# Kernel tuning notes

Hardware: AMD Instinct MI355X
Metric: run time of the kernel (lower is better)

## Reference

```python
import jax, jax.numpy as jnp
import numpy as np

N_NODES = 100000
N_EDGES = 3200000
N_GRAPHS = 4096
BN_EPS = 1e-5


def setup_inputs() -> dict:
    key = jax.random.key(0)
    ks = iter(jax.random.split(key, 64))
    d = {}
    d["x"] = jax.random.normal(next(ks), (N_NODES, 36), dtype=jnp.float32)
    d["edge_index"] = jax.random.randint(next(ks), (2, N_EDGES), 0, N_NODES, dtype=jnp.int32)
    d["batch"] = jnp.sort(jax.random.randint(next(ks), (N_NODES,), 0, N_GRAPHS, dtype=jnp.int32))
    d["num_graphs"] = N_GRAPHS
    # GCN layers: (in, out) per hidden_dims=[128,128,64]
    dims = [(36, 128), (128, 128), (128, 64)]
    for i, (di, do) in enumerate(dims):
        d[f"w{i}"] = jax.random.normal(next(ks), (di, do), dtype=jnp.float32) * (1.0 / np.sqrt(di))
        d[f"b{i}"] = jax.random.normal(next(ks), (do,), dtype=jnp.float32) * 0.01
        d[f"g{i}"] = jax.random.uniform(next(ks), (do,), dtype=jnp.float32, minval=0.5, maxval=1.5)
        d[f"be{i}"] = jax.random.normal(next(ks), (do,), dtype=jnp.float32) * 0.01
        d[f"m{i}"] = jax.random.normal(next(ks), (do,), dtype=jnp.float32) * 0.01
        d[f"v{i}"] = jax.random.uniform(next(ks), (do,), dtype=jnp.float32, minval=0.5, maxval=1.5)
    # FC head: 64 -> 128 -> 64 -> 2
    d["fw0"] = jax.random.normal(next(ks), (64, 128), dtype=jnp.float32) * (1.0 / 8.0)
    d["fb0"] = jax.random.normal(next(ks), (128,), dtype=jnp.float32) * 0.01
    d["fw1"] = jax.random.normal(next(ks), (128, 64), dtype=jnp.float32) * (1.0 / np.sqrt(128))
    d["fb1"] = jax.random.normal(next(ks), (64,), dtype=jnp.float32) * 0.01
    d["ow"] = jax.random.normal(next(ks), (64, 2), dtype=jnp.float32) * (1.0 / 8.0)
    d["ob"] = jax.random.normal(next(ks), (2,), dtype=jnp.float32) * 0.01
    return d


def _gcn_layer(x, w, b, src, dst, norm_e, norm_self, n_nodes):
    # PyG GCNConv with self-loops: out[i] = sum_j norm_ij * (x_j @ W) + b
    xw = x @ w                                   # [N, out]
    msg = xw[src] * norm_e[:, None]              # gather + scale, [E, out]
    agg = jax.ops.segment_sum(msg, dst, num_segments=n_nodes)
    return agg + xw * norm_self[:, None] + b     # self-loop contribution + bias


def _bn_eval(x, g, be, m, v):
    return g * (x - m) * jax.lax.rsqrt(v + BN_EPS) + be


def reference(x, edge_index, batch, num_graphs,
              w0, b0, g0, be0, m0, v0,
              w1, b1, g1, be1, m1, v1,
              w2, b2, g2, be2, m2, v2,
              fw0, fb0, fw1, fb1, ow, ob):
    n = x.shape[0]
    src, dst = edge_index[0], edge_index[1]
    # symmetric GCN normalization with self-loops (gcn_norm)
    deg = jax.ops.segment_sum(jnp.ones(src.shape[0], x.dtype), dst, num_segments=n) + 1.0
    dinv = jax.lax.rsqrt(deg)
    norm_e = dinv[src] * dinv[dst]   # per-edge coeff
    norm_self = dinv * dinv          # self-loop coeff = 1/deg

    params = [(w0, b0, g0, be0, m0, v0), (w1, b1, g1, be1, m1, v1), (w2, b2, g2, be2, m2, v2)]
    h = x
    for (w, b, g, be, m, v) in params:
        h = _gcn_layer(h, w, b, src, dst, norm_e, norm_self, n)
        h = jax.nn.relu(_bn_eval(h, g, be, m, v))  # dropout inactive in eval

    # global mean pool over graphs
    sums = jax.ops.segment_sum(h, batch, num_segments=num_graphs)          # [G, 64]
    cnt = jax.ops.segment_sum(jnp.ones(n, h.dtype), batch, num_segments=num_graphs)
    pooled = sums / jnp.maximum(cnt, 1.0)[:, None]

    h = jax.nn.relu(pooled @ fw0 + fb0)
    h = jax.nn.relu(h @ fw1 + fb1)
    return h @ ow + ob
```

## Files before the change

kernel.cpp:

```cpp
#include <hip/hip_runtime.h>
#include <hip/hip_fp16.h>

#define BN_EPS 1e-5f

#define BUCK_SHIFT 9
#define NBUCK_MAX 256
#define BCAP 20480
#define PBLK 512

typedef _Float16 f16x8 __attribute__((ext_vector_type(8)));
typedef float f32x4 __attribute__((ext_vector_type(4)));

__global__ __launch_bounds__(256) void fused_scatter(const int* __restrict__ src,
                                                     const int* __restrict__ dst,
                                                     int* __restrict__ gcnt,
                                                     int2* __restrict__ ebuf,
                                                     int nE, int nbuck, int chunk) {
    __shared__ int h[NBUCK_MAX], rbase[NBUCK_MAX], cur[NBUCK_MAX];
    const int blk = blockIdx.x, tid = threadIdx.x;
    for (int j = tid; j < nbuck; j += 256) { h[j] = 0; cur[j] = 0; }
    __syncthreads();
    const int base = blk * chunk;
    const int end = min(base + chunk, nE);
    for (int i = base + tid; i < end; i += 256)
        atomicAdd(&h[dst[i] >> BUCK_SHIFT], 1);
    __syncthreads();
    for (int j = tid; j < nbuck; j += 256)
        rbase[j] = h[j] ? atomicAdd(&gcnt[j], h[j]) : 0;
    __syncthreads();
    for (int i = base + tid; i < end; i += 256) {
        int s = src[i], d = dst[i];
        int b = d >> BUCK_SHIFT;
        int p = rbase[b] + atomicAdd(&cur[b], 1);
        if (p < BCAP) ebuf[(size_t)b * BCAP + p] = make_int2(s, d);
    }
}

__global__ __launch_bounds__(256) void fused_csr(const int2* __restrict__ ebuf,
                                                 const int* __restrict__ gcnt,
                                                 const float* __restrict__ x,
                                                 const int* __restrict__ batch,
                                                 int* __restrict__ degI,
                                                 float* __restrict__ dinv,
                                                 int* __restrict__ row_start,
                                                 int* __restrict__ src_sorted,
                                                 __half* __restrict__ xs_h,
                                                 float* __restrict__ cnt, int n) {
    __shared__ int deg[512];
    __shared__ int cur[512];
    __shared__ float sdi[512];
    __shared__ int tmp[256];
    __shared__ int s_low_total;
    const int b = blockIdx.x, tid = threadIdx.x;
    const int nb = b << BUCK_SHIFT;
    const int cntb = min(gcnt[b], BCAP);
    const int2* __restrict__ eb = ebuf + (size_t)b * BCAP;

    for (int j = tid; j < 512; j += 256) deg[j] = 0;
    __syncthreads();
    for (int i = tid; i < cntb; i += 256)
        atomicAdd(&deg[eb[i].y - nb], 1);
    __syncthreads();

    for (int j = tid; j < 512; j += 256) {
        int node = nb + j;
        if (node < n) {
            int d = deg[j];
            degI[node] = d;
            float di = rsqrtf((float)d + 1.0f);
            dinv[node] = di;
            sdi[j] = di;
        }
    }

    int v0 = deg[tid];
    tmp[tid] = v0;
    __syncthreads();
    for (int off = 1; off < 256; off <<= 1) {
        int t = (tid >= off) ? tmp[tid - off] : 0;
        __syncthreads();
        tmp[tid] += t;
        __syncthreads();
    }
    int ex_low = tmp[tid] - v0;
    if (tid == 255) s_low_total = tmp[255];
    __syncthreads();
    int low_total = s_low_total;
    int v1 = deg[256 + tid];
    __syncthreads();
    tmp[tid] = v1;
    __syncthreads();
    for (int off = 1; off < 256; off <<= 1) {
        int t = (tid >= off) ? tmp[tid - off] : 0;
        __syncthreads();
        tmp[tid] += t;
        __syncthreads();
    }
    int ex_high = tmp[tid] - v1 + low_total;

    const int gbase = b * BCAP;
    if (nb + tid < n) row_start[nb + tid] = gbase + ex_low;
    if (nb + 256 + tid < n) row_start[nb + 256 + tid] = gbase + ex_high;
    cur[tid] = ex_low;
    cur[256 + tid] = ex_high;
    __syncthreads();

    for (int i = tid; i < cntb; i += 256) {
        int2 ed = eb[i];
        int p = atomicAdd(&cur[ed.y - nb], 1);
        src_sorted[gbase + p] = ed.x;
    }

    for (int idx = tid; idx < 512 * 18; idx += 256) {
        int j = idx / 18;
        int node = nb + j;
        if (node < n) {
            int c = idx - j * 18;
            float2 v = *(const float2*)(x + (size_t)node * 36 + 2 * c);
            float di = sdi[j];
            *(__half2*)(xs_h + (size_t)node * 36 + 2 * c) = __floats2half2_rn(v.x * di, v.y * di);
        }
    }

    for (int j = tid; j < 512; j += 256) {
        int node = nb + j;
        if (node < n) unsafeAtomicAdd(&cnt[batch[node]], 1.0f);
    }
}

__global__ __launch_bounds__(256) void repack_w(const float* __restrict__ w0,
                                                const float* __restrict__ w1,
                                                const float* __restrict__ w2,
                                                __half* __restrict__ Wp0,
                                                __half* __restrict__ Wp1,
                                                __half* __restrict__ Wp2) {
    const int tid = threadIdx.x;
    if (blockIdx.x == 0) {
        for (int idx = tid; idx < 8 * 4 * 64 * 8; idx += 256) {
            int j = idx & 7, lane = (idx >> 3) & 63, kb = (idx >> 9) & 3, nt = idx >> 11;
            int k = kb * 32 + (lane >> 4) * 8 + j, c = nt * 16 + (lane & 15);
            Wp1[idx] = __float2half_rn(w1[k * 128 + c]);
        }
    } else if (blockIdx.x == 1) {
        for (int idx = tid; idx < 4 * 4 * 64 * 8; idx += 256) {
            int j = idx & 7, lane = (idx >> 3) & 63, kb = (idx >> 9) & 3, nt = idx >> 11;
            int k = kb * 32 + (lane >> 4) * 8 + j, c = nt * 16 + (lane & 15);
            Wp2[idx] = __float2half_rn(w2[k * 64 + c]);
        }
    } else {
        for (int idx = tid; idx < 8 * 2 * 64 * 8; idx += 256) {
            int j = idx & 7, lane = (idx >> 3) & 63, kb = (idx >> 9) & 1, nt = idx >> 10;
            int k = kb * 32 + (lane >> 4) * 8 + j, c = nt * 16 + (lane & 15);
            Wp0[idx] = (k < 36) ? __float2half_rn(w0[k * 128 + c]) : __float2half_rn(0.0f);
        }
    }
}

template<int LDK, int KB, int OUT, int NT, bool BNRELU, bool SCALEOUT>
__global__ __launch_bounds__(256) void gemm_mfma(const __half* __restrict__ in,
                                                 const __half* __restrict__ Wp,
                                                 const float* __restrict__ bias,
                                                 const float* __restrict__ gg,
                                                 const float* __restrict__ bb,
                                                 const float* __restrict__ mm,
                                                 const float* __restrict__ vv,
                                                 const float* __restrict__ dscale,
                                                 __half* __restrict__ out, int n) {
    const int lane = threadIdx.x & 63;
    const int wave = threadIdx.x >> 6;
    const int r0 = blockIdx.x * 64 + wave * 16;
    const int arow = r0 + (lane & 15);
    const int kg = lane >> 4;

    f16x8 a[KB];
#pragma unroll
    for (int kb = 0; kb < KB; kb++)
        a[kb] = *(const f16x8*)(in + (size_t)arow * LDK + kb * 32 + kg * 8);

    f32x4 acc[NT];
#pragma unroll
    for (int nt = 0; nt < NT; nt++) {
        f32x4 z = {0.0f, 0.0f, 0.0f, 0.0f};
        acc[nt] = z;
    }

#pragma unroll
    for (int nt = 0; nt < NT; nt++) {
#pragma unroll
        for (int kb = 0; kb < KB; kb++) {
            f16x8 b = *(const f16x8*)(Wp + ((size_t)(nt * KB + kb) * 64 + lane) * 8);
            acc[nt] = __builtin_amdgcn_mfma_f32_16x16x32_f16(a[kb], b, acc[nt], 0, 0, 0);
        }
    }

    const int col = lane & 15;
    const int rbase = r0 + kg * 4;
    float ds[4] = {1.f, 1.f, 1.f, 1.f};
    if constexpr (SCALEOUT) {
#pragma unroll
        for (int r = 0; r < 4; r++) ds[r] = dscale[rbase + r];
    }
#pragma unroll
    for (int nt = 0; nt < NT; nt++) {
        const int c = nt * 16 + col;
        float s = 1.f, t = 0.f;
        if constexpr (BNRELU) {
            s = gg[c] * rsqrtf(vv[c] + BN_EPS);
            t = bb[c] + (bias[c] - mm[c]) * s;
        }
#pragma unroll
        for (int r = 0; r < 4; r++) {
            float val = acc[nt][r];
            if constexpr (BNRELU) val = fmaxf(val * s + t, 0.0f);
            if constexpr (SCALEOUT) val *= ds[r];
            out[(size_t)(rbase + r) * OUT + c] = __float2half_rn(val);
        }
    }
}

__global__ __launch_bounds__(256) void agg_pull36w_h(const __half* __restrict__ xs_h,
                                                     const int* __restrict__ row_start,
                                                     const int* __restrict__ degI,
                                                     const int* __restrict__ src_sorted,
                                                     const float* __restrict__ dinv,
                                                     __half* __restrict__ out, int n) {
    int node = __builtin_amdgcn_readfirstlane((int)(blockIdx.x * 4 + (threadIdx.x >> 6)));
    if (node >= n) return;
    const int lane = threadIdx.x & 63;
    int e = row_start[node];
    const int re = e + degI[node];
    const float di = dinv[node];

    const char* __restrict__ xb = (const char*)xs_h;
    const unsigned loff = (unsigned)lane << 2;

    float2 acc = make_float2(0.f, 0.f);
    if (lane < 18) acc = __half22float2(*(const __half2*)(xb + ((unsigned)node * 72u + loff)));

    for (; e + 3 < re; e += 4) {
        int s0 = src_sorted[e], s1 = src_sorted[e + 1],
            s2 = src_sorted[e + 2], s3 = src_sorted[e + 3];
        if (lane < 18) {
            float2 a0 = __half22float2(*(const __half2*)(xb + ((unsigned)s0 * 72u + loff)));
            float2 a1 = __half22float2(*(const __half2*)(xb + ((unsigned)s1 * 72u + loff)));
            float2 a2 = __half22float2(*(const __half2*)(xb + ((unsigned)s2 * 72u + loff)));
            float2 a3 = __half22float2(*(const __half2*)(xb + ((unsigned)s3 * 72u + loff)));
            acc.x += (a0.x + a1.x) + (a2.x + a3.x);
            acc.y += (a0.y + a1.y) + (a2.y + a3.y);
        }
    }
    for (; e < re; e++) {
        int s = src_sorted[e];
        if (lane < 18) {
            float2 a = __half22float2(*(const __half2*)(xb + ((unsigned)s * 72u + loff)));
            acc.x += a.x;
            acc.y += a.y;
        }
    }
    if (lane < 32) {
        __half2 o = __floats2half2_rn(acc.x * di, acc.y * di);
        *(__half2*)((char*)out + (((unsigned)node << 7) + loff)) = o;
    }
}

__global__ __launch_bounds__(256) void agg_pull_wave2_h(const __half* __restrict__ feat_h,
                                                        const int* __restrict__ row_start,
                                                        const int* __restrict__ degI,
                                                        const int* __restrict__ src_sorted,
                                                        const float* __restrict__ dinv,
                                                        __half* __restrict__ out, int n) {
    int node = __builtin_amdgcn_readfirstlane((int)(blockIdx.x * 4 + (threadIdx.x >> 6)));
    if (node >= n) return;
    const int lane = threadIdx.x & 63;
    int e = row_start[node];
    const int re = e + degI[node];
    const float di = dinv[node];

    const char* __restrict__ fb = (const char*)feat_h;
    const unsigned loff = (unsigned)lane << 2;

    float2 acc = __half22float2(*(const __half2*)(fb + (((unsigned)node << 8) + loff)));

    for (; e + 3 < re; e += 4) {
        int s0 = src_sorted[e], s1 = src_sorted[e + 1],
            s2 = src_sorted[e + 2], s3 = src_sorted[e + 3];
        float2 a0 = __half22float2(*(const __half2*)(fb + (((unsigned)s0 << 8) + loff)));
        float2 a1 = __half22float2(*(const __half2*)(fb + (((unsigned)s1 << 8) + loff)));
        float2 a2 = __half22float2(*(const __half2*)(fb + (((unsigned)s2 << 8) + loff)));
        float2 a3 = __half22float2(*(const __half2*)(fb + (((unsigned)s3 << 8) + loff)));
        acc.x += (a0.x + a1.x) + (a2.x + a3.x);
        acc.y += (a0.y + a1.y) + (a2.y + a3.y);
    }
    for (; e < re; e++) {
        int s = src_sorted[e];
        float2 a = __half22float2(*(const __half2*)(fb + (((unsigned)s << 8) + loff)));
        acc.x += a.x;
        acc.y += a.y;
    }
    __half2 o = __floats2half2_rn(acc.x * di, acc.y * di);
    *(__half2*)((char*)out + (((unsigned)node << 8) + loff)) = o;
}

__global__ __launch_bounds__(256) void agg_pull_pool_h(const __half* __restrict__ feat_h,
                                                       const int* __restrict__ row_start,
                                                       const int* __restrict__ degI,
                                                       const int* __restrict__ src_sorted,
                                                       const float* __restrict__ dinv,
                                                       const float* __restrict__ bias,
                                                       const float* __restrict__ gg,
                                                       const float* __restrict__ bb,
                                                       const float* __restrict__ mm,
                                                       const float* __restrict__ vv,
                                                       const int* __restrict__ batch,
                                                       float* __restrict__ pool, int n) {
    int node = __builtin_amdgcn_readfirstlane((int)(blockIdx.x * 4 + (threadIdx.x >> 6)));
    if (node >= n) return;
    const int lane = threadIdx.x & 63;
    int e = row_start[node];
    const int re = e + degI[node];
    const float di = dinv[node];

    const char* __restrict__ fb = (const char*)feat_h;
    const unsigned loff = (unsigned)lane << 1;

    float acc = __half2float(*(const __half*)(fb + (((unsigned)node << 7) + loff)));

    for (; e + 3 < re; e += 4) {
        int s0 = src_sorted[e], s1 = src_sorted[e + 1],
            s2 = src_sorted[e + 2], s3 = src_sorted[e + 3];
        float a0 = __half2float(*(const __half*)(fb + (((unsigned)s0 << 7) + loff)));
        float a1 = __half2float(*(const __half*)(fb + (((unsigned)s1 << 7) + loff)));
        float a2 = __half2float(*(const __half*)(fb + (((unsigned)s2 << 7) + loff)));
        float a3 = __half2float(*(const __half*)(fb + (((unsigned)s3 << 7) + loff)));
        acc += (a0 + a1) + (a2 + a3);
    }
    for (; e < re; e++) {
        acc += __half2float(*(const __half*)(fb + (((unsigned)src_sorted[e] << 7) + loff)));
    }
    float h = acc * di + bias[lane];
    float scale = gg[lane] * rsqrtf(vv[lane] + BN_EPS);
    float val = fmaxf((h - mm[lane]) * scale + bb[lane], 0.0f);
    unsafeAtomicAdd(&pool[(size_t)batch[node] * 64 + lane], val);
}

__global__ __launch_bounds__(128) void fc_head_kernel(const float* __restrict__ pool,
                                                      const float* __restrict__ cnt,
                                                      const float* __restrict__ fw0,
                                                      const float* __restrict__ fb0,
                                                      const float* __restrict__ fw1,
                                                      const float* __restrict__ fb1,
                                                      const float* __restrict__ ow,
                                                      const float* __restrict__ ob,
                                                      float* __restrict__ out) {
    int g = blockIdx.x, tid = threadIdx.x;
    __shared__ float p[64], h1[128], h2[64];
    if (tid < 64) p[tid] = pool[g * 64 + tid] / fmaxf(cnt[g], 1.0f);
    __syncthreads();
    {
        float acc = fb0[tid];
        for (int k = 0; k < 64; k++) acc += p[k] * fw0[k * 128 + tid];
        h1[tid] = fmaxf(acc, 0.0f);
    }
    __syncthreads();
    if (tid < 64) {
        float acc = fb1[tid];
        for (int k = 0; k < 128; k++) acc += h1[k] * fw1[k * 64 + tid];
        h2[tid] = fmaxf(acc, 0.0f);
    }
    __syncthreads();
    if (tid < 2) {
        float acc = ob[tid];
        for (int k = 0; k < 64; k++) acc += h2[k] * ow[k * 2 + tid];
        out[g * 2 + tid] = acc;
    }
}

extern "C" void kernel_launch(void* const* d_in, const int* in_sizes, int n_in,
                              void* d_out, int out_size, void* d_ws, size_t ws_size,
                              hipStream_t stream) {
    const float* x     = (const float*)d_in[0];
    const int*   eidx  = (const int*)d_in[1];
    const int*   batch = (const int*)d_in[2];
    const float* w0 = (const float*)d_in[4];
    const float* b0 = (const float*)d_in[5];
    const float* g0 = (const float*)d_in[6];
    const float* be0 = (const float*)d_in[7];
    const float* m0 = (const float*)d_in[8];
    const float* v0 = (const float*)d_in[9];
    const float* w1 = (const float*)d_in[10];
    const float* b1 = (const float*)d_in[11];
    const float* g1 = (const float*)d_in[12];
    const float* be1 = (const float*)d_in[13];
    const float* m1 = (const float*)d_in[14];
    const float* v1 = (const float*)d_in[15];
    const float* w2 = (const float*)d_in[16];
    const float* b2 = (const float*)d_in[17];
    const float* g2 = (const float*)d_in[18];
    const float* be2 = (const float*)d_in[19];
    const float* m2 = (const float*)d_in[20];
    const float* v2 = (const float*)d_in[21];
    const float* fw0 = (const float*)d_in[22];
    const float* fb0 = (const float*)d_in[23];
    const float* fw1 = (const float*)d_in[24];
    const float* fb1 = (const float*)d_in[25];
    const float* ow = (const float*)d_in[26];
    const float* ob = (const float*)d_in[27];

    const int N = in_sizes[0] / 36;
    const int E = in_sizes[1] / 2;
    const int G = out_size / 2;
    const int* src = eidx;
    const int* dst = eidx + E;

    const int nbuck = (N + 511) >> BUCK_SHIFT;
    const int chunk = (E + PBLK - 1) / PBLK;
    const int NPAD = ((N + 63) / 64) * 64;
    const int NGP = NPAD / 64;

    char* wsb = (char*)d_ws;
    int2*   ebuf       = (int2*)wsb;    wsb += (size_t)nbuck * BCAP * 8;
    __half* F1         = (__half*)wsb;  wsb += (size_t)NPAD * 128 * 2;
    __half* F1a        = (__half*)wsb;  wsb += (size_t)NPAD * 128 * 2;
    __half* F2         = (__half*)wsb;  wsb += (size_t)NPAD * 64 * 2;
    __half* A36h       = (__half*)wsb;  wsb += (size_t)NPAD * 64 * 2;
    __half* xs_h       = (__half*)wsb;  wsb += (size_t)N * 36 * 2;
    int*    src_sorted = (int*)wsb;     wsb += (size_t)nbuck * BCAP * 4;
    int*    degI       = (int*)wsb;     wsb += (size_t)N * 4;
    int*    row_start  = (int*)wsb;     wsb += (size_t)N * 4;
    float*  dinv       = (float*)wsb;   wsb += (size_t)NPAD * 4;
    float*  pool       = (float*)wsb;   wsb += (size_t)G * 64 * 4;
    float*  cnt        = (float*)wsb;   wsb += (size_t)G * 4;
    int*    gcnt       = (int*)wsb;     wsb += 256 * 4;
    __half* Wp0        = (__half*)wsb;  wsb += 8192 * 2;
    __half* Wp1        = (__half*)wsb;  wsb += 16384 * 2;
    __half* Wp2        = (__half*)wsb;  wsb += 8192 * 2;
    __half* F1b        = (__half*)ebuf;

    hipMemsetAsync(gcnt, 0, 256 * 4, stream);
    hipMemsetAsync(pool, 0, (size_t)G * 64 * 4, stream);
    hipMemsetAsync(cnt, 0, (size_t)G * 4, stream);
    repack_w<<<3, 256, 0, stream>>>(w0, w1, w2, Wp0, Wp1, Wp2);

    fused_scatter<<<PBLK, 256, 0, stream>>>(src, dst, gcnt, ebuf, E, nbuck, chunk);
    fused_csr<<<nbuck, 256, 0, stream>>>(ebuf, gcnt, x, batch, degI, dinv, row_start,
                                         src_sorted, xs_h, cnt, N);

    const int NW = (N + 3) / 4;

    agg_pull36w_h<<<NW, 256, 0, stream>>>(xs_h, row_start, degI, src_sorted, dinv, A36h, N);
    gemm_mfma<64, 2, 128, 8, true, true><<<NGP, 256, 0, stream>>>(
        A36h, Wp0, b0, g0, be0, m0, v0, dinv, F1, N);

    agg_pull_wave2_h<<<NW, 256, 0, stream>>>(F1, row_start, degI, src_sorted, dinv, F1a, N);
    gemm_mfma<128, 4, 128, 8, true, false><<<NGP, 256, 0, stream>>>(
        F1a, Wp1, b1, g1, be1, m1, v1, nullptr, F1b, N);

    gemm_mfma<128, 4, 64, 4, false, true><<<NGP, 256, 0, stream>>>(
        F1b, Wp2, nullptr, nullptr, nullptr, nullptr, nullptr, dinv, F2, N);

    agg_pull_pool_h<<<NW, 256, 0, stream>>>(
        F2, row_start, degI, src_sorted, dinv, b2, g2, be2, m2, v2, batch, pool, N);

    fc_head_kernel<<<G, 128, 0, stream>>>(pool, cnt, fw0, fb0, fw1, fb1, ow, ob, (float*)d_out);
}
```

Before: 576.5 us.

## Fuse layer-1/2 GEMMs, pack edge buffer to 32-bit, merge prep memsets

Merges the layer-1 GEMM (with BN+ReLU) and the layer-2 GEMM into one kernel that keeps the intermediate 16x128 tile per wave in LDS, so the F1b round trip through global memory and one launch go away. The bucketed edge buffer now packs the local destination (9 bits) and the source (17 bits) into one int, which halves scatter write and CSR read traffic. The three memsets and the weight repack become a single prep kernel. Packing assumes node ids fit in 17 bits (N < 131072), which holds for this input size.

```diff
diff --git a/kernel.cpp b/kernel.cpp
--- a/kernel.cpp
+++ b/kernel.cpp
@@ -11,10 +11,50 @@
 typedef _Float16 f16x8 __attribute__((ext_vector_type(8)));
 typedef float f32x4 __attribute__((ext_vector_type(4)));
 
+__global__ __launch_bounds__(256) void prep0(const float* __restrict__ w0,
+                                             const float* __restrict__ w1,
+                                             const float* __restrict__ w2,
+                                             __half* __restrict__ Wp0,
+                                             __half* __restrict__ Wp1,
+                                             __half* __restrict__ Wp2,
+                                             int* __restrict__ gcnt,
+                                             float* __restrict__ pool,
+                                             float* __restrict__ cnt, int G) {
+    const int tid = threadIdx.x;
+    if (blockIdx.x == 0) {
+        for (int idx = tid; idx < 8 * 4 * 64 * 8; idx += 256) {
+            int j = idx & 7, lane = (idx >> 3) & 63, kb = (idx >> 9) & 3, nt = idx >> 11;
+            int k = kb * 32 + (lane >> 4) * 8 + j, c = nt * 16 + (lane & 15);
+            Wp1[idx] = __float2half_rn(w1[k * 128 + c]);
+        }
+    } else if (blockIdx.x == 1) {
+        for (int idx = tid; idx < 4 * 4 * 64 * 8; idx += 256) {
+            int j = idx & 7, lane = (idx >> 3) & 63, kb = (idx >> 9) & 3, nt = idx >> 11;
+            int k = kb * 32 + (lane >> 4) * 8 + j, c = nt * 16 + (lane & 15);
+            Wp2[idx] = __float2half_rn(w2[k * 64 + c]);
+        }
+    } else if (blockIdx.x == 2) {
+        for (int idx = tid; idx < 8 * 2 * 64 * 8; idx += 256) {
+            int j = idx & 7, lane = (idx >> 3) & 63, kb = (idx >> 9) & 1, nt = idx >> 10;
+            int k = kb * 32 + (lane >> 4) * 8 + j, c = nt * 16 + (lane & 15);
+            Wp0[idx] = (k < 36) ? __float2half_rn(w0[k * 128 + c]) : __float2half_rn(0.0f);
+        }
+    } else {
+        const int zb = blockIdx.x - 3;
+        const int nzb = gridDim.x - 3;
+        const int tot = G * 64 + G + 256;
+        for (int i = zb * 256 + tid; i < tot; i += nzb * 256) {
+            if (i < G * 64) pool[i] = 0.0f;
+            else if (i < G * 64 + G) cnt[i - G * 64] = 0.0f;
+            else gcnt[i - G * 64 - G] = 0;
+        }
+    }
+}
+
 __global__ __launch_bounds__(256) void fused_scatter(const int* __restrict__ src,
                                                      const int* __restrict__ dst,
                                                      int* __restrict__ gcnt,
-                                                     int2* __restrict__ ebuf,
+                                                     int* __restrict__ ebuf,
                                                      int nE, int nbuck, int chunk) {
     __shared__ int h[NBUCK_MAX], rbase[NBUCK_MAX], cur[NBUCK_MAX];
     const int blk = blockIdx.x, tid = threadIdx.x;
@@ -32,11 +72,11 @@
         int s = src[i], d = dst[i];
         int b = d >> BUCK_SHIFT;
         int p = rbase[b] + atomicAdd(&cur[b], 1);
-        if (p < BCAP) ebuf[(size_t)b * BCAP + p] = make_int2(s, d);
-    }
-}
-
-__global__ __launch_bounds__(256) void fused_csr(const int2* __restrict__ ebuf,
+        if (p < BCAP) ebuf[(size_t)b * BCAP + p] = ((d & 511) << 17) | s;
+    }
+}
+
+__global__ __launch_bounds__(256) void fused_csr(const int* __restrict__ ebuf,
                                                  const int* __restrict__ gcnt,
                                                  const float* __restrict__ x,
                                                  const int* __restrict__ batch,
@@ -54,12 +94,12 @@
     const int b = blockIdx.x, tid = threadIdx.x;
     const int nb = b << BUCK_SHIFT;
     const int cntb = min(gcnt[b], BCAP);
-    const int2* __restrict__ eb = ebuf + (size_t)b * BCAP;
+    const int* __restrict__ eb = ebuf + (size_t)b * BCAP;
 
     for (int j = tid; j < 512; j += 256) deg[j] = 0;
     __syncthreads();
     for (int i = tid; i < cntb; i += 256)
-        atomicAdd(&deg[eb[i].y - nb], 1);
+        atomicAdd(&deg[((unsigned)eb[i]) >> 17], 1);
     __syncthreads();
 
     for (int j = tid; j < 512; j += 256) {
@@ -106,9 +146,9 @@
     __syncthreads();
 
     for (int i = tid; i < cntb; i += 256) {
-        int2 ed = eb[i];
-        int p = atomicAdd(&cur[ed.y - nb], 1);
-        src_sorted[gbase + p] = ed.x;
+        unsigned ed = (unsigned)eb[i];
+        int p = atomicAdd(&cur[ed >> 17], 1);
+        src_sorted[gbase + p] = (int)(ed & 0x1FFFFu);
     }
 
     for (int idx = tid; idx < 512 * 18; idx += 256) {
@@ -125,34 +165,6 @@
     for (int j = tid; j < 512; j += 256) {
         int node = nb + j;
         if (node < n) unsafeAtomicAdd(&cnt[batch[node]], 1.0f);
-    }
-}
-
-__global__ __launch_bounds__(256) void repack_w(const float* __restrict__ w0,
-                                                const float* __restrict__ w1,
-                                                const float* __restrict__ w2,
-                                                __half* __restrict__ Wp0,
-                                                __half* __restrict__ Wp1,
-                                                __half* __restrict__ Wp2) {
-    const int tid = threadIdx.x;
-    if (blockIdx.x == 0) {
-        for (int idx = tid; idx < 8 * 4 * 64 * 8; idx += 256) {
-            int j = idx & 7, lane = (idx >> 3) & 63, kb = (idx >> 9) & 3, nt = idx >> 11;
-            int k = kb * 32 + (lane >> 4) * 8 + j, c = nt * 16 + (lane & 15);
-            Wp1[idx] = __float2half_rn(w1[k * 128 + c]);
-        }
-    } else if (blockIdx.x == 1) {
-        for (int idx = tid; idx < 4 * 4 * 64 * 8; idx += 256) {
-            int j = idx & 7, lane = (idx >> 3) & 63, kb = (idx >> 9) & 3, nt = idx >> 11;
-            int k = kb * 32 + (lane >> 4) * 8 + j, c = nt * 16 + (lane & 15);
-            Wp2[idx] = __float2half_rn(w2[k * 64 + c]);
-        }
-    } else {
-        for (int idx = tid; idx < 8 * 2 * 64 * 8; idx += 256) {
-            int j = idx & 7, lane = (idx >> 3) & 63, kb = (idx >> 9) & 1, nt = idx >> 10;
-            int k = kb * 32 + (lane >> 4) * 8 + j, c = nt * 16 + (lane & 15);
-            Wp0[idx] = (k < 36) ? __float2half_rn(w0[k * 128 + c]) : __float2half_rn(0.0f);
-        }
     }
 }
 
@@ -215,6 +227,89 @@
             if constexpr (SCALEOUT) val *= ds[r];
             out[(size_t)(rbase + r) * OUT + c] = __float2half_rn(val);
         }
+    }
+}
+
+__global__ __launch_bounds__(256) void gemm12_mfma(const __half* __restrict__ in,
+                                                   const __half* __restrict__ Wp1,
+                                                   const float* __restrict__ b1,
+                                                   const float* __restrict__ g1,
+                                                   const float* __restrict__ be1,
+                                                   const float* __restrict__ m1,
+                                                   const float* __restrict__ v1,
+                                                   const __half* __restrict__ Wp2,
+                                                   const float* __restrict__ dscale,
+                                                   __half* __restrict__ out, int n) {
+    __shared__ __align__(16) _Float16 s_h[4][16][136];
+    const int lane = threadIdx.x & 63;
+    const int wave = threadIdx.x >> 6;
+    const int r0 = blockIdx.x * 64 + wave * 16;
+    const int arow = r0 + (lane & 15);
+    const int kg = lane >> 4;
+    const int col = lane & 15;
+
+    f16x8 a[4];
+#pragma unroll
+    for (int kb = 0; kb < 4; kb++)
+        a[kb] = *(const f16x8*)(in + (size_t)arow * 128 + kb * 32 + kg * 8);
+
+    f32x4 acc1[8];
+#pragma unroll
+    for (int nt = 0; nt < 8; nt++) {
+        f32x4 z = {0.0f, 0.0f, 0.0f, 0.0f};
+        acc1[nt] = z;
+    }
+#pragma unroll
+    for (int nt = 0; nt < 8; nt++) {
+#pragma unroll
+        for (int kb = 0; kb < 4; kb++) {
+            f16x8 b = *(const f16x8*)(Wp1 + ((size_t)(nt * 4 + kb) * 64 + lane) * 8);
+            acc1[nt] = __builtin_amdgcn_mfma_f32_16x16x32_f16(a[kb], b, acc1[nt], 0, 0, 0);
+        }
+    }
+
+#pragma unroll
+    for (int nt = 0; nt < 8; nt++) {
+        const int c = nt * 16 + col;
+        float s = g1[c] * rsqrtf(v1[c] + BN_EPS);
+        float t = be1[c] + (b1[c] - m1[c]) * s;
+#pragma unroll
+        for (int r = 0; r < 4; r++) {
+            float val = fmaxf(acc1[nt][r] * s + t, 0.0f);
+            s_h[wave][kg * 4 + r][c] = (_Float16)val;
+        }
+    }
+
+    f16x8 a2[4];
+#pragma unroll
+    for (int kb = 0; kb < 4; kb++)
+        a2[kb] = *(const f16x8*)&s_h[wave][col][kb * 32 + kg * 8];
+
+    f32x4 acc2[4];
+#pragma unroll
+    for (int nt = 0; nt < 4; nt++) {
+        f32x4 z = {0.0f, 0.0f, 0.0f, 0.0f};
+        acc2[nt] = z;
+    }
+#pragma unroll
+    for (int nt = 0; nt < 4; nt++) {
+#pragma unroll
+        for (int kb = 0; kb < 4; kb++) {
+            f16x8 b = *(const f16x8*)(Wp2 + ((size_t)(nt * 4 + kb) * 64 + lane) * 8);
+            acc2[nt] = __builtin_amdgcn_mfma_f32_16x16x32_f16(a2[kb], b, acc2[nt], 0, 0, 0);
+        }
+    }
+
+    const int rbase = r0 + kg * 4;
+    float ds[4];
+#pragma unroll
+    for (int r = 0; r < 4; r++) ds[r] = dscale[rbase + r];
+#pragma unroll
+    for (int nt = 0; nt < 4; nt++) {
+        const int c = nt * 16 + col;
+#pragma unroll
+        for (int r = 0; r < 4; r++)
+            out[(size_t)(rbase + r) * 64 + c] = __float2half_rn(acc2[nt][r] * ds[r]);
     }
 }
 
@@ -418,7 +513,7 @@
     const int NGP = NPAD / 64;
 
     char* wsb = (char*)d_ws;
-    int2*   ebuf       = (int2*)wsb;    wsb += (size_t)nbuck * BCAP * 8;
+    int*    ebuf       = (int*)wsb;     wsb += (size_t)nbuck * BCAP * 4;
     __half* F1         = (__half*)wsb;  wsb += (size_t)NPAD * 128 * 2;
     __half* F1a        = (__half*)wsb;  wsb += (size_t)NPAD * 128 * 2;
     __half* F2         = (__half*)wsb;  wsb += (size_t)NPAD * 64 * 2;
@@ -434,12 +529,8 @@
     __half* Wp0        = (__half*)wsb;  wsb += 8192 * 2;
     __half* Wp1        = (__half*)wsb;  wsb += 16384 * 2;
     __half* Wp2        = (__half*)wsb;  wsb += 8192 * 2;
-    __half* F1b        = (__half*)ebuf;
-
-    hipMemsetAsync(gcnt, 0, 256 * 4, stream);
-    hipMemsetAsync(pool, 0, (size_t)G * 64 * 4, stream);
-    hipMemsetAsync(cnt, 0, (size_t)G * 4, stream);
-    repack_w<<<3, 256, 0, stream>>>(w0, w1, w2, Wp0, Wp1, Wp2);
+
+    prep0<<<64, 256, 0, stream>>>(w0, w1, w2, Wp0, Wp1, Wp2, gcnt, pool, cnt, G);
 
     fused_scatter<<<PBLK, 256, 0, stream>>>(src, dst, gcnt, ebuf, E, nbuck, chunk);
     fused_csr<<<nbuck, 256, 0, stream>>>(ebuf, gcnt, x, batch, degI, dinv, row_start,
@@ -452,11 +543,7 @@
         A36h, Wp0, b0, g0, be0, m0, v0, dinv, F1, N);
 
     agg_pull_wave2_h<<<NW, 256, 0, stream>>>(F1, row_start, degI, src_sorted, dinv, F1a, N);
-    gemm_mfma<128, 4, 128, 8, true, false><<<NGP, 256, 0, stream>>>(
-        F1a, Wp1, b1, g1, be1, m1, v1, nullptr, F1b, N);
-
-    gemm_mfma<128, 4, 64, 4, false, true><<<NGP, 256, 0, stream>>>(
-        F1b, Wp2, nullptr, nullptr, nullptr, nullptr, nullptr, dinv, F2, N);
+    gemm12_mfma<<<NGP, 256, 0, stream>>>(F1a, Wp1, b1, g1, be1, m1, v1, Wp2, dinv, F2, N);
 
     agg_pull_pool_h<<<NW, 256, 0, stream>>>(
         F2, row_start, degI, src_sorted, dinv, b2, g2, be2, m2, v2, batch, pool, N);
```

After: 552.5 us, median of 2. -4.2%, faster.
